# Optimization experiments

Measured on AMD Instinct MI355X. Metric: run time of the kernel, lower is better.

The kernel has to match this reference:

```python
import jax, jax.numpy as jnp
import numpy as np

N = 1024          # number of junctions
H = 1024          # heatmap height
W = 1024          # heatmap width
NUM_SAMPLES = 64  # samples along each candidate segment (torch_sampler)
DETECT_THRESH = 0.5
INLIER_THRESH = 0.99


def setup_inputs() -> dict:
    key = jax.random.key(0)
    k1, k2 = jax.random.split(key)
    # junctions are (h, w) float coordinates inside the image
    junctions = jax.random.uniform(k1, (N, 2), dtype=jnp.float32) * (H - 1)
    heatmap = jax.random.uniform(k2, (H, W), dtype=jnp.float32)
    return {"junctions": junctions, "heatmap": heatmap}


def _bilinear_sample(heatmap, ch, cw):
    """SOLD2 detect_bilinear: gather 4 corners, bilinear weights. ch/cw: [N,N,S]."""
    hf = jnp.floor(ch); hc = jnp.ceil(ch)
    wf = jnp.floor(cw); wc = jnp.ceil(cw)
    hfi = hf.astype(jnp.int32); hci = hc.astype(jnp.int32)
    wfi = wf.astype(jnp.int32); wci = wc.astype(jnp.int32)
    return (heatmap[hfi, wfi] * (hc - ch) * (wc - cw)
          + heatmap[hfi, wci] * (hc - ch) * (cw - wf)
          + heatmap[hci, wfi] * (ch - hf) * (wc - cw)
          + heatmap[hci, wci] * (ch - hf) * (cw - wf))


def reference(junctions, heatmap):
    n = junctions.shape[0]
    Hh, Ww = heatmap.shape
    t = jnp.linspace(0.0, 1.0, NUM_SAMPLES, dtype=jnp.float32)  # [S]
    # cand_samples[i, j, s] = junc[i] * t[s] + junc[j] * (1 - t[s])  (start=i, end=j)
    ch = junctions[:, None, 0:1] * t + junctions[None, :, 0:1] * (1.0 - t)  # [N,N,S]
    cw = junctions[:, None, 1:2] * t + junctions[None, :, 1:2] * (1.0 - t)  # [N,N,S]
    ch = jnp.clip(ch, 0.0, Hh - 1)
    cw = jnp.clip(cw, 0.0, Ww - 1)
    feat = _bilinear_sample(heatmap, ch, cw)                    # [N,N,S]
    mean_feat = feat.mean(axis=-1)                              # [N,N]
    inlier_ratio = (feat > DETECT_THRESH).astype(jnp.float32).mean(axis=-1)
    # candidate map: strict upper triangle (torch.triu(ones, diagonal=1))
    cand_mask = jnp.triu(jnp.ones((n, n), dtype=bool), k=1)
    detected = (mean_feat > DETECT_THRESH) & (inlier_ratio >= INLIER_THRESH) & cand_mask
    line_map = (detected | detected.T).astype(jnp.int32)        # symmetric line map
    return line_map, mean_feat
```

## Files before the change

### kernel.cpp

```cpp
#include <hip/hip_runtime.h>

#define NJ 1024
#define DETECT 0.5f
#define RESCUE 0.4975f

__device__ __forceinline__ float sample_t(int s) {
    return (s == 63) ? 1.0f : (float)s * (1.0f / 63.0f);
}

__device__ __forceinline__ int tiled_idx(int h, int w) {
    return ((h >> 2) << 12) + ((w >> 2) << 4) + ((h & 3) << 2) + (w & 3);
}

__device__ __forceinline__ void exact_pair(const float2 ja, const float2 jb,
                                           const float* __restrict__ heat,
                                           float& mean_o, float& min_o)
{
    float acc = 0.0f;
    float mn  = __builtin_inff();
    for (int s = 0; s < 64; ++s) {
        const float t  = sample_t(s);
        const float om = 1.0f - t;
        float ch = __fadd_rn(__fmul_rn(ja.x, t), __fmul_rn(jb.x, om));
        float cw = __fadd_rn(__fmul_rn(ja.y, t), __fmul_rn(jb.y, om));
        ch = fminf(fmaxf(ch, 0.0f), 1023.0f);
        cw = fminf(fmaxf(cw, 0.0f), 1023.0f);
        const float hf = floorf(ch), hc = ceilf(ch);
        const float wf = floorf(cw), wc = ceilf(cw);
        const int hfi = (int)hf, hci = (int)hc;
        const int wfi = (int)wf, wci = (int)wc;
        const float a00 = heat[(hfi << 10) + wfi];
        const float a01 = heat[(hfi << 10) + wci];
        const float a10 = heat[(hci << 10) + wfi];
        const float a11 = heat[(hci << 10) + wci];
        const float t1 = __fmul_rn(__fmul_rn(a00, __fsub_rn(hc, ch)), __fsub_rn(wc, cw));
        const float t2 = __fmul_rn(__fmul_rn(a01, __fsub_rn(hc, ch)), __fsub_rn(cw, wf));
        const float t3 = __fmul_rn(__fmul_rn(a10, __fsub_rn(ch, hf)), __fsub_rn(wc, cw));
        const float t4 = __fmul_rn(__fmul_rn(a11, __fsub_rn(ch, hf)), __fsub_rn(cw, wf));
        const float feat = __fadd_rn(__fadd_rn(__fadd_rn(t1, t2), t3), t4);
        acc += feat;
        mn = fminf(mn, feat);
    }
    mean_o = acc * (1.0f / 64.0f);
    min_o  = mn;
}

__device__ __forceinline__ unsigned int expand_bits16(unsigned int v) {
    v &= 0x0000FFFFu;
    v = (v | (v << 8)) & 0x00FF00FFu;
    v = (v | (v << 4)) & 0x0F0F0F0Fu;
    v = (v | (v << 2)) & 0x33333333u;
    v = (v | (v << 1)) & 0x55555555u;
    return v;
}

__global__ __launch_bounds__(256) void prep_kernel(
    const float* __restrict__ junc, const float* __restrict__ heat,
    unsigned int* __restrict__ packed, float2* __restrict__ sortedJ,
    int* __restrict__ perm)
{
    const int b = blockIdx.x;
    if (b < 256) {
        const int idx = (b << 8) + threadIdx.x;
        const int th = idx >> 8;
        const int tw = idx & 255;
        const int h0 = th << 2;
        const int w0 = tw << 2;

        float v[5][5];
        #pragma unroll
        for (int a = 0; a < 5; ++a) {
            const int h = (h0 + a <= 1023) ? h0 + a : 1023;
            const float* row = heat + (h << 10);
            const float4 f4 = *(const float4*)(row + w0);
            v[a][0] = f4.x; v[a][1] = f4.y; v[a][2] = f4.z; v[a][3] = f4.w;
            const int w4 = (w0 + 4 <= 1023) ? w0 + 4 : 1023;
            v[a][4] = row[w4];
        }

        unsigned int q[5][5];
        #pragma unroll
        for (int a = 0; a < 5; ++a)
            #pragma unroll
            for (int c = 0; c < 5; ++c)
                q[a][c] = (unsigned int)__float2int_rn(v[a][c] * 255.0f);

        unsigned int out[16];
        #pragma unroll
        for (int a = 0; a < 4; ++a)
            #pragma unroll
            for (int c = 0; c < 4; ++c)
                out[(a << 2) + c] = q[a][c] | (q[a][c + 1] << 8)
                                  | (q[a + 1][c] << 16) | (q[a + 1][c + 1] << 24);

        uint4* dst = (uint4*)(packed + ((th << 12) + (tw << 4)));
        dst[0] = make_uint4(out[0],  out[1],  out[2],  out[3]);
        dst[1] = make_uint4(out[4],  out[5],  out[6],  out[7]);
        dst[2] = make_uint4(out[8],  out[9],  out[10], out[11]);
        dst[3] = make_uint4(out[12], out[13], out[14], out[15]);
    } else {
        __shared__ unsigned int keys[1024];
        const int t = threadIdx.x;
        unsigned int mykey[4];
        #pragma unroll
        for (int m = 0; m < 4; ++m) {
            const int i = (m << 8) + t;
            const float2 jc2 = ((const float2*)junc)[i];
            const int mh = min(max((int)jc2.x, 0), 1023);
            const int mw = min(max((int)jc2.y, 0), 1023);
            const unsigned int mort = (expand_bits16((unsigned int)mh) << 1)
                                    |  expand_bits16((unsigned int)mw);
            mykey[m] = (mort << 10) | (unsigned int)i;
            keys[i] = mykey[m];
        }
        __syncthreads();
        int rank[4] = {0, 0, 0, 0};
        for (int k = 0; k < 1024; ++k) {
            const unsigned int kk = keys[k];
            #pragma unroll
            for (int m = 0; m < 4; ++m) rank[m] += (kk < mykey[m]) ? 1 : 0;
        }
        #pragma unroll
        for (int m = 0; m < 4; ++m) {
            const int i = (m << 8) + t;
            perm[rank[m]] = i;
            sortedJ[rank[m]] = ((const float2*)junc)[i];
        }
    }
}

__global__ __launch_bounds__(256) void sold2_thread_kernel(
    const float2* __restrict__ sortedJ,
    const int* __restrict__ perm,
    const float* __restrict__ heat,
    const unsigned int* __restrict__ packed,
    float* __restrict__ line_out,
    float* __restrict__ mean_out)
{
    const int q = blockIdx.x * 256 + threadIdx.x;
    const int r = q / 513;
    const int c = q - r * 513;
    const int jc = (r + c) & 1023;

    const float2 jr = sortedJ[r];
    const float2 jj = sortedJ[jc];

    float acc = 0.0f;
    float mn  = __builtin_inff();

    #pragma unroll
    for (int s0 = 0; s0 < 64; s0 += 16) {
        float chv[16], cwv[16];
        unsigned int cv[16];
        #pragma unroll
        for (int u = 0; u < 16; ++u) {
            const int s = s0 + u;
            const float t  = sample_t(s);
            const float om = 1.0f - t;
            float ch = __fadd_rn(__fmul_rn(jr.x, t), __fmul_rn(jj.x, om));
            float cw = __fadd_rn(__fmul_rn(jr.y, t), __fmul_rn(jj.y, om));
            ch = fminf(fmaxf(ch, 0.0f), 1023.0f);
            cw = fminf(fmaxf(cw, 0.0f), 1023.0f);
            chv[u] = ch;
            cwv[u] = cw;
            const int hfi = (int)ch;
            const int wfi = (int)cw;
            cv[u] = packed[tiled_idx(hfi, wfi)];
        }
        #pragma unroll
        for (int u = 0; u < 16; ++u) {
            const float ch = chv[u], cw = cwv[u];
            const float hf = floorf(ch), hc = ceilf(ch);
            const float wf = floorf(cw), wc = ceilf(cw);
            const float wh0 = hc - ch, wh1 = ch - hf;
            const float ww0 = wc - cw, ww1 = cw - wf;
            const unsigned int cc = cv[u];
            const float a00 = (float)(cc & 0xffu);
            const float a01 = (float)((cc >> 8) & 0xffu);
            const float a10 = (float)((cc >> 16) & 0xffu);
            const float a11 = (float)(cc >> 24);
            const float feat = a00 * (wh0 * ww0) + a01 * (wh0 * ww1)
                             + a10 * (wh1 * ww0) + a11 * (wh1 * ww1);
            acc += feat;
            mn = fminf(mn, feat);
        }
    }

    float mean = acc * (1.0f / (255.0f * 64.0f));
    const float mns = mn * (1.0f / 255.0f);

    bool det = false;
    if ((mns > RESCUE) && (mean > RESCUE) && (c != 0)) {
        float mn2;
        exact_pair(jr, jj, heat, mean, mn2);
        det = (mean > DETECT) && (mn2 > DETECT);
    }

    const int io = perm[r];
    const int jo = perm[jc];
    const float lv = det ? 1.0f : 0.0f;

    const int p1 = (io << 10) + jo;
    __builtin_nontemporal_store(mean, mean_out + p1);
    __builtin_nontemporal_store(lv,   line_out + p1);

    if (c != 0 && c != 512) {
        const int p2 = (jo << 10) + io;
        __builtin_nontemporal_store(mean, mean_out + p2);
        __builtin_nontemporal_store(lv,   line_out + p2);
    }
}

extern "C" void kernel_launch(void* const* d_in, const int* in_sizes, int n_in,
                              void* d_out, int out_size, void* d_ws, size_t ws_size,
                              hipStream_t stream) {
    const float* junc = (const float*)d_in[0];
    const float* heat = (const float*)d_in[1];
    float* line_out = (float*)d_out;
    float* mean_out = line_out + NJ * NJ;

    unsigned int* packed = (unsigned int*)d_ws;
    float2* sortedJ = (float2*)((char*)d_ws + (4u << 20));
    int* perm = (int*)((char*)d_ws + (4u << 20) + 8192);

    prep_kernel<<<257, 256, 0, stream>>>(junc, heat, packed, sortedJ, perm);

    const int total = NJ * 513;
    sold2_thread_kernel<<<total / 256, 256, 0, stream>>>(sortedJ, perm, heat,
                                                         packed, line_out, mean_out);
}
```

Measured before the change: 185.6 us.

## Replace rank-count sort with bitonic sort and move diagonal pairs to prep kernel

The single-block O(N^2) rank-counting Morton sort becomes a 1024-thread shared-memory bitonic sort in its own kernel. Diagonal (i,i) pairs are now computed exactly in extra blocks of the packing kernel, so the main kernel covers exactly 512 columns per row. That lets it use shift and mask indexing instead of division by 513 and drops the c==0 special cases. The change adds a third kernel launch, and the diagonal work is done with the slower exact path on unquantized data.

Measured after the change: 193.0 us. 4.0% more time.

```diff
diff --git a/kernel.cpp b/kernel.cpp
--- a/kernel.cpp
+++ b/kernel.cpp
@@ -54,10 +54,10 @@
     return v;
 }
 
-__global__ __launch_bounds__(256) void prep_kernel(
+__global__ __launch_bounds__(256) void pack_diag_kernel(
     const float* __restrict__ junc, const float* __restrict__ heat,
-    unsigned int* __restrict__ packed, float2* __restrict__ sortedJ,
-    int* __restrict__ perm)
+    unsigned int* __restrict__ packed, float* __restrict__ line_out,
+    float* __restrict__ mean_out)
 {
     const int b = blockIdx.x;
     if (b < 256) {
@@ -99,34 +99,47 @@
         dst[2] = make_uint4(out[8],  out[9],  out[10], out[11]);
         dst[3] = make_uint4(out[12], out[13], out[14], out[15]);
     } else {
-        __shared__ unsigned int keys[1024];
-        const int t = threadIdx.x;
-        unsigned int mykey[4];
-        #pragma unroll
-        for (int m = 0; m < 4; ++m) {
-            const int i = (m << 8) + t;
-            const float2 jc2 = ((const float2*)junc)[i];
-            const int mh = min(max((int)jc2.x, 0), 1023);
-            const int mw = min(max((int)jc2.y, 0), 1023);
-            const unsigned int mort = (expand_bits16((unsigned int)mh) << 1)
-                                    |  expand_bits16((unsigned int)mw);
-            mykey[m] = (mort << 10) | (unsigned int)i;
-            keys[i] = mykey[m];
-        }
-        __syncthreads();
-        int rank[4] = {0, 0, 0, 0};
-        for (int k = 0; k < 1024; ++k) {
-            const unsigned int kk = keys[k];
-            #pragma unroll
-            for (int m = 0; m < 4; ++m) rank[m] += (kk < mykey[m]) ? 1 : 0;
-        }
-        #pragma unroll
-        for (int m = 0; m < 4; ++m) {
-            const int i = (m << 8) + t;
-            perm[rank[m]] = i;
-            sortedJ[rank[m]] = ((const float2*)junc)[i];
-        }
-    }
+        const int i = ((b - 256) << 8) + threadIdx.x;
+        const float2 ji = ((const float2*)junc)[i];
+        float mean, mn;
+        exact_pair(ji, ji, heat, mean, mn);
+        mean_out[(i << 10) + i] = mean;
+        line_out[(i << 10) + i] = 0.0f;
+    }
+}
+
+__global__ __launch_bounds__(1024) void sort_kernel(
+    const float* __restrict__ junc, float2* __restrict__ sortedJ,
+    int* __restrict__ perm)
+{
+    __shared__ unsigned int sk[1024];
+    __shared__ unsigned short sv[1024];
+    const int t = threadIdx.x;
+    const float2 jc = ((const float2*)junc)[t];
+    const int mh = min(max((int)jc.x, 0), 1023);
+    const int mw = min(max((int)jc.y, 0), 1023);
+    sk[t] = (expand_bits16((unsigned int)mh) << 1) | expand_bits16((unsigned int)mw);
+    sv[t] = (unsigned short)t;
+    __syncthreads();
+
+    for (unsigned int k = 2; k <= 1024; k <<= 1) {
+        for (unsigned int s = k >> 1; s > 0; s >>= 1) {
+            const int l = t ^ (int)s;
+            if (l > t) {
+                const unsigned int a = sk[t], b = sk[l];
+                const bool up = ((t & k) == 0);
+                if ((a > b) == up) {
+                    sk[t] = b; sk[l] = a;
+                    const unsigned short va = sv[t];
+                    sv[t] = sv[l]; sv[l] = va;
+                }
+            }
+            __syncthreads();
+        }
+    }
+    const int src = (int)sv[t];
+    perm[t] = src;
+    sortedJ[t] = ((const float2*)junc)[src];
 }
 
 __global__ __launch_bounds__(256) void sold2_thread_kernel(
@@ -138,8 +151,8 @@
     float* __restrict__ mean_out)
 {
     const int q = blockIdx.x * 256 + threadIdx.x;
-    const int r = q / 513;
-    const int c = q - r * 513;
+    const int r = q >> 9;
+    const int c = 1 + (q & 511);
     const int jc = (r + c) & 1023;
 
     const float2 jr = sortedJ[r];
@@ -190,7 +203,7 @@
     const float mns = mn * (1.0f / 255.0f);
 
     bool det = false;
-    if ((mns > RESCUE) && (mean > RESCUE) && (c != 0)) {
+    if ((mns > RESCUE) && (mean > RESCUE)) {
         float mn2;
         exact_pair(jr, jj, heat, mean, mn2);
         det = (mean > DETECT) && (mn2 > DETECT);
@@ -204,7 +217,7 @@
     __builtin_nontemporal_store(mean, mean_out + p1);
     __builtin_nontemporal_store(lv,   line_out + p1);
 
-    if (c != 0 && c != 512) {
+    if (c != 512) {
         const int p2 = (jo << 10) + io;
         __builtin_nontemporal_store(mean, mean_out + p2);
         __builtin_nontemporal_store(lv,   line_out + p2);
@@ -223,9 +236,10 @@
     float2* sortedJ = (float2*)((char*)d_ws + (4u << 20));
     int* perm = (int*)((char*)d_ws + (4u << 20) + 8192);
 
-    prep_kernel<<<257, 256, 0, stream>>>(junc, heat, packed, sortedJ, perm);
-
-    const int total = NJ * 513;
+    pack_diag_kernel<<<260, 256, 0, stream>>>(junc, heat, packed, line_out, mean_out);
+    sort_kernel<<<1, 1024, 0, stream>>>(junc, sortedJ, perm);
+
+    const int total = NJ * 512;
     sold2_thread_kernel<<<total / 256, 256, 0, stream>>>(sortedJ, perm, heat,
                                                          packed, line_out, mean_out);
 }
```

## Replace O(n²) rank sort with coarse counting sort; move diagonal pairs to prep

Applied to the files above, without the earlier changes.

Swaps the 1024×1024 comparison-rank sort in the prep block for a counting sort on a coarse 32×32 Morton cell key, built from shared atomics and a prefix scan. This removes a serial single-block bottleneck that likely dominated prep time. The diagonal (i,i) pairs are now computed exactly by four extra prep blocks, so the main kernel indexes with shifts instead of division by 513 and launches exactly 512 pairs per row. The trade-off is that the coarse key gives a non-deterministic ordering within cells, which may slightly reduce sample locality in the main kernel.

New measurement: 180.1 us. 3.0% less time.

```diff
diff --git a/kernel.cpp b/kernel.cpp
--- a/kernel.cpp
+++ b/kernel.cpp
@@ -57,11 +57,62 @@
 __global__ __launch_bounds__(256) void prep_kernel(
     const float* __restrict__ junc, const float* __restrict__ heat,
     unsigned int* __restrict__ packed, float2* __restrict__ sortedJ,
-    int* __restrict__ perm)
+    int* __restrict__ perm, float* __restrict__ line_out,
+    float* __restrict__ mean_out)
 {
+    __shared__ unsigned int cnt[1024];
+    __shared__ unsigned int base[1024];
+    __shared__ unsigned int wtot[4];
+
     const int b = blockIdx.x;
-    if (b < 256) {
-        const int idx = (b << 8) + threadIdx.x;
+    if (b == 0) {
+        const int t = threadIdx.x;
+        #pragma unroll
+        for (int m = 0; m < 4; ++m) cnt[(m << 8) + t] = 0u;
+        __syncthreads();
+
+        unsigned int key[4], slot[4];
+        #pragma unroll
+        for (int m = 0; m < 4; ++m) {
+            const int i = (m << 8) + t;
+            const float2 jc2 = ((const float2*)junc)[i];
+            const unsigned int mh = (unsigned int)(min(max((int)jc2.x, 0), 1023) >> 5);
+            const unsigned int mw = (unsigned int)(min(max((int)jc2.y, 0), 1023) >> 5);
+            key[m] = (expand_bits16(mh) << 1) | expand_bits16(mw);
+            slot[m] = atomicAdd(&cnt[key[m]], 1u);
+        }
+        __syncthreads();
+
+        unsigned int c4[4];
+        unsigned int tsum = 0;
+        #pragma unroll
+        for (int u = 0; u < 4; ++u) { c4[u] = cnt[(t << 2) + u]; tsum += c4[u]; }
+        unsigned int scan = tsum;
+        #pragma unroll
+        for (int off = 1; off < 64; off <<= 1) {
+            const unsigned int n = __shfl_up(scan, off, 64);
+            if ((t & 63) >= off) scan += n;
+        }
+        if ((t & 63) == 63) wtot[t >> 6] = scan;
+        __syncthreads();
+        unsigned int wbase = 0;
+        for (int wv = 0; wv < (t >> 6); ++wv) wbase += wtot[wv];
+        const unsigned int ex = wbase + scan - tsum;
+        base[(t << 2) + 0] = ex;
+        base[(t << 2) + 1] = ex + c4[0];
+        base[(t << 2) + 2] = ex + c4[0] + c4[1];
+        base[(t << 2) + 3] = ex + c4[0] + c4[1] + c4[2];
+        __syncthreads();
+
+        #pragma unroll
+        for (int m = 0; m < 4; ++m) {
+            const int i = (m << 8) + t;
+            const unsigned int pos = base[key[m]] + slot[m];
+            perm[pos] = i;
+            sortedJ[pos] = ((const float2*)junc)[i];
+        }
+    } else if (b <= 256) {
+        const int idx = ((b - 1) << 8) + threadIdx.x;
         const int th = idx >> 8;
         const int tw = idx & 255;
         const int h0 = th << 2;
@@ -99,33 +150,12 @@
         dst[2] = make_uint4(out[8],  out[9],  out[10], out[11]);
         dst[3] = make_uint4(out[12], out[13], out[14], out[15]);
     } else {
-        __shared__ unsigned int keys[1024];
-        const int t = threadIdx.x;
-        unsigned int mykey[4];
-        #pragma unroll
-        for (int m = 0; m < 4; ++m) {
-            const int i = (m << 8) + t;
-            const float2 jc2 = ((const float2*)junc)[i];
-            const int mh = min(max((int)jc2.x, 0), 1023);
-            const int mw = min(max((int)jc2.y, 0), 1023);
-            const unsigned int mort = (expand_bits16((unsigned int)mh) << 1)
-                                    |  expand_bits16((unsigned int)mw);
-            mykey[m] = (mort << 10) | (unsigned int)i;
-            keys[i] = mykey[m];
-        }
-        __syncthreads();
-        int rank[4] = {0, 0, 0, 0};
-        for (int k = 0; k < 1024; ++k) {
-            const unsigned int kk = keys[k];
-            #pragma unroll
-            for (int m = 0; m < 4; ++m) rank[m] += (kk < mykey[m]) ? 1 : 0;
-        }
-        #pragma unroll
-        for (int m = 0; m < 4; ++m) {
-            const int i = (m << 8) + t;
-            perm[rank[m]] = i;
-            sortedJ[rank[m]] = ((const float2*)junc)[i];
-        }
+        const int i = ((b - 257) << 8) + threadIdx.x;
+        const float2 ji = ((const float2*)junc)[i];
+        float mean, mn;
+        exact_pair(ji, ji, heat, mean, mn);
+        mean_out[(i << 10) + i] = mean;
+        line_out[(i << 10) + i] = 0.0f;
     }
 }
 
@@ -138,8 +168,8 @@
     float* __restrict__ mean_out)
 {
     const int q = blockIdx.x * 256 + threadIdx.x;
-    const int r = q / 513;
-    const int c = q - r * 513;
+    const int r = q >> 9;
+    const int c = 1 + (q & 511);
     const int jc = (r + c) & 1023;
 
     const float2 jr = sortedJ[r];
@@ -190,7 +220,7 @@
     const float mns = mn * (1.0f / 255.0f);
 
     bool det = false;
-    if ((mns > RESCUE) && (mean > RESCUE) && (c != 0)) {
+    if ((mns > RESCUE) && (mean > RESCUE)) {
         float mn2;
         exact_pair(jr, jj, heat, mean, mn2);
         det = (mean > DETECT) && (mn2 > DETECT);
@@ -204,7 +234,7 @@
     __builtin_nontemporal_store(mean, mean_out + p1);
     __builtin_nontemporal_store(lv,   line_out + p1);
 
-    if (c != 0 && c != 512) {
+    if (c != 512) {
         const int p2 = (jo << 10) + io;
         __builtin_nontemporal_store(mean, mean_out + p2);
         __builtin_nontemporal_store(lv,   line_out + p2);
@@ -223,9 +253,10 @@
     float2* sortedJ = (float2*)((char*)d_ws + (4u << 20));
     int* perm = (int*)((char*)d_ws + (4u << 20) + 8192);
 
-    prep_kernel<<<257, 256, 0, stream>>>(junc, heat, packed, sortedJ, perm);
-
-    const int total = NJ * 513;
+    prep_kernel<<<261, 256, 0, stream>>>(junc, heat, packed, sortedJ, perm,
+                                         line_out, mean_out);
+
+    const int total = NJ * 512;
     sold2_thread_kernel<<<total / 256, 256, 0, stream>>>(sortedJ, perm, heat,
                                                          packed, line_out, mean_out);
 }
```
